# Optimization experiments

Measured on AMD Instinct MI355X. Metric: run time of the kernel, lower is better.

Reference implementation:

```python
import jax, jax.numpy as jnp
import numpy as np

B, C, H, W = 8, 512, 64, 64
K = 8  # shrink factor: qk channels = C//K, v channels = C//2


def conv1x1(x, w, b):
    # x: [B,C_in,H,W], w: [C_out,C_in], b: [C_out]  (1x1 conv == channel matmul)
    return jnp.einsum('bchw,oc->bohw', x, w) + b[None, :, None, None]


def maxpool2x2(x):
    b, c, h, w = x.shape
    return x.reshape(b, c, h // 2, 2, w // 2, 2).max(axis=(3, 5))


def setup_inputs() -> dict:
    key = jax.random.key(0)
    ks = jax.random.split(key, 9)
    Cqk, Cv = C // K, C // 2
    sc = lambda fan_in: 1.0 / np.sqrt(fan_in)
    return {
        'x': jax.random.normal(ks[0], (B, C, H, W), jnp.float32),
        'Wf': jax.random.normal(ks[1], (Cqk, C), jnp.float32) * sc(C),
        'bf': jnp.zeros((Cqk,), jnp.float32),
        'Wg': jax.random.normal(ks[2], (Cqk, C), jnp.float32) * sc(C),
        'bg': jnp.zeros((Cqk,), jnp.float32),
        'Wh': jax.random.normal(ks[3], (Cv, C), jnp.float32) * sc(C),
        'bh': jnp.zeros((Cv,), jnp.float32),
        'Wv': jax.random.normal(ks[4], (C, Cv), jnp.float32) * sc(Cv),
        'bv': jnp.zeros((C,), jnp.float32),
        'gamma': jnp.float32(0.5),
    }


def reference(x, Wf, bf, Wg, bg, Wh, bh, Wv, bv, gamma):
    b, c, h, w = x.shape
    f = conv1x1(x, Wf, bf).reshape(b, c // K, h * w)          # [B, C/K, HW]
    g = maxpool2x2(conv1x1(x, Wg, bg))                         # [B, C/K, H/2, W/2]
    v = maxpool2x2(conv1x1(x, Wh, bh))                         # [B, C/2, H/2, W/2]
    hwp = (h // 2) * (w // 2)
    g = g.reshape(b, c // K, hwp)
    v = v.reshape(b, c // 2, hwp)
    # s[b, n, m] = sum_c f[b,c,n] g[b,c,m]; softmax over m (no scaling, per SAGAN)
    s = jnp.einsum('bcn,bcm->bnm', f, g)                       # [B, HW, HW']
    beta = jax.nn.softmax(s, axis=-1)
    o = jnp.einsum('bcm,bnm->bcn', v, beta).reshape(b, c // 2, h, w)
    return gamma * conv1x1(o, Wv, bv) + x
```

## Files before the change

kernel.cpp:

```cpp
#include <hip/hip_runtime.h>
#include <cstddef>

typedef __attribute__((ext_vector_type(4))) float f32x4;
typedef __attribute__((ext_vector_type(16))) float f32x16;
typedef __attribute__((ext_vector_type(8))) short bf16x8;

#define MFMA16(A, B, C) __builtin_amdgcn_mfma_f32_16x16x32_bf16(A, B, C, 0, 0, 0)
#define MFMA32(A, B, C) __builtin_amdgcn_mfma_f32_32x32x16_bf16(A, B, C, 0, 0, 0)

__device__ __forceinline__ unsigned short f2bf(float f) {
  unsigned u = __float_as_uint(f);
  u += 0x7fffu + ((u >> 16) & 1u);
  return (unsigned short)(u >> 16);
}
__device__ __forceinline__ float bf2f(unsigned short s) {
  return __uint_as_float(((unsigned)s) << 16);
}

__device__ __forceinline__ void cvt_split8(float4 a, float4 b, bf16x8* H, bf16x8* L) {
  float v[8] = {a.x, a.y, a.z, a.w, b.x, b.y, b.z, b.w};
  unsigned hh[4], ll[4];
  #pragma unroll
  for (int p = 0; p < 4; ++p) {
    unsigned short h0 = f2bf(v[2 * p]), h1 = f2bf(v[2 * p + 1]);
    hh[p] = (unsigned)h0 | ((unsigned)h1 << 16);
    unsigned short l0 = f2bf(v[2 * p] - bf2f(h0));
    unsigned short l1 = f2bf(v[2 * p + 1] - bf2f(h1));
    ll[p] = (unsigned)l0 | ((unsigned)l1 << 16);
  }
  uint4 uh; uh.x = hh[0]; uh.y = hh[1]; uh.z = hh[2]; uh.w = hh[3];
  uint4 ul; ul.x = ll[0]; ul.y = ll[1]; ul.z = ll[2]; ul.w = ll[3];
  *H = *(bf16x8*)&uh;
  *L = *(bf16x8*)&ul;
}

__device__ __forceinline__ bf16x8 cvt_hi8(float4 a, float4 b) {
  float v[8] = {a.x, a.y, a.z, a.w, b.x, b.y, b.z, b.w};
  unsigned hh[4];
  #pragma unroll
  for (int p = 0; p < 4; ++p)
    hh[p] = (unsigned)f2bf(v[2 * p]) | ((unsigned)f2bf(v[2 * p + 1]) << 16);
  uint4 uh; uh.x = hh[0]; uh.y = hh[1]; uh.z = hh[2]; uh.w = hh[3];
  return *(bf16x8*)&uh;
}


__global__ void prep_k(const float* __restrict__ Wf, const float* __restrict__ Wg,
                       const float* __restrict__ Wh, const float* __restrict__ Wv,
                       unsigned short* __restrict__ wfh, unsigned short* __restrict__ wfl,
                       unsigned short* __restrict__ wgh, unsigned short* __restrict__ wgl,
                       unsigned short* __restrict__ whb, unsigned short* __restrict__ wvb) {
  int i = blockIdx.x * 256 + threadIdx.x;
  if (i < 65536) {
    int ii = i & 32767;
    int j = ii & 7, slot = (ii >> 3) & 63, q = slot & 15, qt2 = slot >> 4;
    int kt = (ii >> 9) & 15, oct = ii >> 13;
    const float* src = (i < 32768) ? Wf : Wg;
    unsigned short* dh = (i < 32768) ? wfh : wgh;
    unsigned short* dl = (i < 32768) ? wfl : wgl;
    float v = src[(oct * 16 + q) * 512 + kt * 32 + qt2 * 8 + j];
    unsigned short h = f2bf(v);
    dh[ii] = h; dl[ii] = f2bf(v - bf2f(h));
  } else if (i < 196608) {
    int ii = i - 65536;
    int j = ii & 7, slot = (ii >> 3) & 63, q = slot & 15, qt2 = slot >> 4;
    int kt = (ii >> 9) & 15, oct = ii >> 13;
    whb[ii] = f2bf(Wh[(oct * 16 + q) * 512 + kt * 32 + qt2 * 8 + j]);
  } else if (i < 327680) {
    int ii = i - 196608;
    int j = ii & 7, slot = (ii >> 3) & 63, q = slot & 15, qt2 = slot >> 4;
    int kt = (ii >> 9) & 7, oct = ii >> 12;
    wvb[ii] = f2bf(Wv[(oct * 16 + q) * 256 + kt * 32 + qt2 * 8 + j]);
  }
}


#define LOADX(CN) { _Pragma("unroll") \
  for (int t_ = 0; t_ < 16; ++t_) vv[t_] = xbase[(size_t)((CN) * 32 + kq + t_) * 4096]; }
#define STOREX(XS) { _Pragma("unroll") \
  for (int i_ = 0; i_ < 4; ++i_) { \
    float4 wv_; wv_.x = vv[4*i_]; wv_.y = vv[4*i_+1]; wv_.z = vv[4*i_+2]; wv_.w = vv[4*i_+3]; \
    *(float4*)&(XS)[nloc][kq + 4 * i_] = wv_; } }

__global__ __launch_bounds__(256, 2)
void conv_all(const float* __restrict__ x,
              const unsigned short* __restrict__ wfh_, const unsigned short* __restrict__ wfl_,
              const unsigned short* __restrict__ wgh_, const unsigned short* __restrict__ wgl_,
              const unsigned short* __restrict__ whb_,
              const float* __restrict__ bf_, const float* __restrict__ bg_,
              const float* __restrict__ bh_,
              unsigned short* __restrict__ fhi, unsigned short* __restrict__ flo,
              unsigned short* __restrict__ ghi, unsigned short* __restrict__ glo,
              unsigned short* __restrict__ vp)
{
  __shared__ __align__(16) char smem[34304];
  float (*xsA)[33] = (float(*)[33])smem;
  float (*xsB)[33] = (float(*)[33])(smem + 16896);
  const int bid = blockIdx.x;
  const int b = bid & 7;
  const int idx = bid >> 3;
  const int role = idx & 1;
  const int hp = idx >> 1;
  const int n0 = hp * 128;
  const int tid = threadIdx.x, w = tid >> 6, lane = tid & 63, q = lane & 15, qt = lane >> 4;
  const int nloc = tid & 127;
  const int kq = (tid >> 7) * 16;
  const float* xbase = x + (size_t)(b * 512) * 4096 + n0 + nloc;
  float vv[16];

  if (role == 0) {
    f32x4 accf[2][4], accg[2][4];
    #pragma unroll
    for (int nt = 0; nt < 2; ++nt)
      #pragma unroll
      for (int ot = 0; ot < 4; ++ot) {
        accf[nt][ot] = (f32x4){0.f, 0.f, 0.f, 0.f};
        accg[nt][ot] = (f32x4){0.f, 0.f, 0.f, 0.f};
      }
    LOADX(0) STOREX(xsA)
    __syncthreads();
    for (int cc = 0; cc < 16; ++cc) {
      float (*cur)[33] = (cc & 1) ? xsB : xsA;
      float (*nxt)[33] = (cc & 1) ? xsA : xsB;
      if (cc < 15) LOADX(cc + 1)
      bf16x8 Ah[2], Al[2];
      #pragma unroll
      for (int nt = 0; nt < 2; ++nt) {
        int row = w * 32 + nt * 16 + q;
        float4 a0 = *(const float4*)&cur[row][qt * 8];
        float4 a1 = *(const float4*)&cur[row][qt * 8 + 4];
        cvt_split8(a0, a1, &Ah[nt], &Al[nt]);
      }
      {
        bf16x8 Bh[4], Bl[4];
        #pragma unroll
        for (int ot = 0; ot < 4; ++ot) {
          size_t wb = ((size_t)(ot * 16 + cc) << 9) + lane * 8;
          Bh[ot] = *(const bf16x8*)(wfh_ + wb);
          Bl[ot] = *(const bf16x8*)(wfl_ + wb);
        }
        #pragma unroll
        for (int nt = 0; nt < 2; ++nt)
          #pragma unroll
          for (int ot = 0; ot < 4; ++ot) {
            accf[nt][ot] = MFMA16(Ah[nt], Bh[ot], accf[nt][ot]);
            accf[nt][ot] = MFMA16(Ah[nt], Bl[ot], accf[nt][ot]);
            accf[nt][ot] = MFMA16(Al[nt], Bh[ot], accf[nt][ot]);
          }
      }
      {
        bf16x8 Bh[4], Bl[4];
        #pragma unroll
        for (int ot = 0; ot < 4; ++ot) {
          size_t wb = ((size_t)(ot * 16 + cc) << 9) + lane * 8;
          Bh[ot] = *(const bf16x8*)(wgh_ + wb);
          Bl[ot] = *(const bf16x8*)(wgl_ + wb);
        }
        #pragma unroll
        for (int nt = 0; nt < 2; ++nt)
          #pragma unroll
          for (int ot = 0; ot < 4; ++ot) {
            accg[nt][ot] = MFMA16(Ah[nt], Bh[ot], accg[nt][ot]);
            accg[nt][ot] = MFMA16(Ah[nt], Bl[ot], accg[nt][ot]);
            accg[nt][ot] = MFMA16(Al[nt], Bh[ot], accg[nt][ot]);
          }
      }
      if (cc < 15) STOREX(nxt)
      __syncthreads();
    }
    #pragma unroll
    for (int nt = 0; nt < 2; ++nt)
      #pragma unroll
      for (int ot = 0; ot < 4; ++ot)
        #pragma unroll
        for (int r = 0; r < 4; ++r) {
          float v = accf[nt][ot][r] + bf_[ot * 16 + q];
          unsigned short h = f2bf(v);
          size_t o = (((size_t)(b * 128 + hp * 4 + w) * 4 + ot) * 64 +
                      (q >> 3) * 32 + nt * 16 + qt * 4 + r) * 8 + (q & 7);
          fhi[o] = h;
          flo[o] = f2bf(v - bf2f(h));
        }
    float (*pl)[67] = (float(*)[67])smem;
    #pragma unroll
    for (int nt = 0; nt < 2; ++nt)
      #pragma unroll
      for (int ot = 0; ot < 4; ++ot)
        #pragma unroll
        for (int r = 0; r < 4; ++r)
          pl[w * 32 + nt * 16 + qt * 4 + r][ot * 16 + q] = accg[nt][ot][r];
    __syncthreads();
    const int c = tid & 63;
    #pragma unroll
    for (int it = 0; it < 8; ++it) {
      int wp = (tid >> 6) + it * 4;
      float v = fmaxf(fmaxf(pl[2 * wp][c], pl[2 * wp + 1][c]),
                      fmaxf(pl[64 + 2 * wp][c], pl[65 + 2 * wp][c])) + bg_[c];
      unsigned short h = f2bf(v);
      size_t o = (((size_t)(b * 32 + hp) * 4 + (c >> 4)) * 64 +
                  ((c >> 3) & 1) * 32 + wp) * 8 + (c & 7);
      ghi[o] = h;
      glo[o] = f2bf(v - bf2f(h));
    }
  } else {
    f32x4 acc[2][16];
    #pragma unroll
    for (int nt = 0; nt < 2; ++nt)
      #pragma unroll
      for (int ot = 0; ot < 16; ++ot) acc[nt][ot] = (f32x4){0.f, 0.f, 0.f, 0.f};
    LOADX(0) STOREX(xsA)
    __syncthreads();
    for (int cc = 0; cc < 16; ++cc) {
      float (*cur)[33] = (cc & 1) ? xsB : xsA;
      float (*nxt)[33] = (cc & 1) ? xsA : xsB;
      if (cc < 15) LOADX(cc + 1)
      bf16x8 A_[2];
      #pragma unroll
      for (int nt = 0; nt < 2; ++nt) {
        int row = w * 32 + nt * 16 + q;
        float4 a0 = *(const float4*)&cur[row][qt * 8];
        float4 a1 = *(const float4*)&cur[row][qt * 8 + 4];
        A_[nt] = cvt_hi8(a0, a1);
      }
      #pragma unroll
      for (int oh = 0; oh < 2; ++oh) {
        bf16x8 B_[8];
        #pragma unroll
        for (int ot = 0; ot < 8; ++ot)
          B_[ot] = *(const bf16x8*)(whb_ + ((size_t)((oh * 8 + ot) * 16 + cc) << 9) + lane * 8);
        #pragma unroll
        for (int nt = 0; nt < 2; ++nt)
          #pragma unroll
          for (int ot = 0; ot < 8; ++ot)
            acc[nt][oh * 8 + ot] = MFMA16(A_[nt], B_[ot], acc[nt][oh * 8 + ot]);
      }
      if (cc < 15) STOREX(nxt)
      __syncthreads();
    }
    float (*pl)[67] = (float(*)[67])smem;
    #pragma unroll
    for (int oh = 0; oh < 4; ++oh) {
      if (oh) __syncthreads();
      #pragma unroll
      for (int nt = 0; nt < 2; ++nt)
        #pragma unroll
        for (int ot4 = 0; ot4 < 4; ++ot4)
          #pragma unroll
          for (int r = 0; r < 4; ++r)
            pl[w * 32 + nt * 16 + qt * 4 + r][ot4 * 16 + q] = acc[nt][oh * 4 + ot4][r];
      __syncthreads();
      const int wp = tid & 31;
      #pragma unroll
      for (int it = 0; it < 8; ++it) {
        int cc2 = (tid >> 5) + it * 8;
        int cv = oh * 64 + cc2;
        float v = fmaxf(fmaxf(pl[2 * wp][cc2], pl[2 * wp + 1][cc2]),
                        fmaxf(pl[64 + 2 * wp][cc2], pl[65 + 2 * wp][cc2])) + bh_[cv];
        size_t o = (((size_t)(b * 16 + (cv >> 4)) * 32 + hp) * 64 +
                    (wp >> 3) * 16 + (cv & 15)) * 8 + (wp & 7);
        vp[o] = f2bf(v);
      }
    }
  }
}


#define PROW 264

__global__ __launch_bounds__(256, 2)
void attn_mfma(const unsigned short* __restrict__ f_, const unsigned short* __restrict__ fl_,
               const unsigned short* __restrict__ g_, const unsigned short* __restrict__ gl_,
               const unsigned short* __restrict__ vp, unsigned short* __restrict__ oT)
{
  __shared__ __align__(16) unsigned short PB[64 * PROW];
  __shared__ float redm[4][2][32], reds[4][2][32];
  __shared__ float rfrow[64], Srow[64];
  const int b = blockIdx.x & 7, bx = blockIdx.x >> 3;
  const int tid = threadIdx.x, w = tid >> 6, lane = tid & 63;
  const int q32 = lane & 31, hl = lane >> 5;
  const int q16 = lane & 15, qt = lane >> 4;

  bf16x8 Fh[2][4], Fl[2][4];
  #pragma unroll
  for (int qt2 = 0; qt2 < 2; ++qt2) {
    size_t fb = ((size_t)(b * 128 + bx * 2 + qt2) << 11) + lane * 8;
    #pragma unroll
    for (int s = 0; s < 4; ++s) {
      Fh[qt2][s] = *(const bf16x8*)(f_ + fb + (s << 9));
      Fl[qt2][s] = *(const bf16x8*)(fl_ + fb + (s << 9));
    }
  }

  float M0 = -3.0e38f, M1 = -3.0e38f;
  f32x4 oacc[4][4];
  #pragma unroll
  for (int c4 = 0; c4 < 4; ++c4)
    #pragma unroll
    for (int qs = 0; qs < 4; ++qs) oacc[c4][qs] = (f32x4){0.f, 0.f, 0.f, 0.f};
  const size_t vroot = ((size_t)(b * 16 + w * 4) * 32) * 512 + lane * 8;

#define VLD(C4, KS) (*(const bf16x8*)(vp + vroot + ((size_t)((C4) * 32 + mc * 8 + (KS)) << 9)))
#define LOADVA(KS) { va0 = VLD(0, KS); va1 = VLD(1, KS); va2 = VLD(2, KS); va3 = VLD(3, KS); }
#define LOADVB(KS) { vb0 = VLD(0, KS); vb1 = VLD(1, KS); vb2 = VLD(2, KS); vb3 = VLD(3, KS); }
#define PVMFMA(KS, V0, V1, V2, V3) { \
  bf16x8 pb0 = *(const bf16x8*)&PB[q16 * PROW + (KS) * 32 + qt * 8]; \
  bf16x8 pb1 = *(const bf16x8*)&PB[(16 + q16) * PROW + (KS) * 32 + qt * 8]; \
  bf16x8 pb2 = *(const bf16x8*)&PB[(32 + q16) * PROW + (KS) * 32 + qt * 8]; \
  bf16x8 pb3 = *(const bf16x8*)&PB[(48 + q16) * PROW + (KS) * 32 + qt * 8]; \
  oacc[0][0] = MFMA16(V0, pb0, oacc[0][0]); oacc[1][0] = MFMA16(V1, pb0, oacc[1][0]); \
  oacc[2][0] = MFMA16(V2, pb0, oacc[2][0]); oacc[3][0] = MFMA16(V3, pb0, oacc[3][0]); \
  oacc[0][1] = MFMA16(V0, pb1, oacc[0][1]); oacc[1][1] = MFMA16(V1, pb1, oacc[1][1]); \
  oacc[2][1] = MFMA16(V2, pb1, oacc[2][1]); oacc[3][1] = MFMA16(V3, pb1, oacc[3][1]); \
  oacc[0][2] = MFMA16(V0, pb2, oacc[0][2]); oacc[1][2] = MFMA16(V1, pb2, oacc[1][2]); \
  oacc[2][2] = MFMA16(V2, pb2, oacc[2][2]); oacc[3][2] = MFMA16(V3, pb2, oacc[3][2]); \
  oacc[0][3] = MFMA16(V0, pb3, oacc[0][3]); oacc[1][3] = MFMA16(V1, pb3, oacc[1][3]); \
  oacc[2][3] = MFMA16(V2, pb3, oacc[2][3]); oacc[3][3] = MFMA16(V3, pb3, oacc[3][3]); }

  #pragma unroll 1
  for (int mc = 0; mc < 4; ++mc) {
    f32x16 sa0t0 = {}, sa0t1 = {}, sa1t0 = {}, sa1t1 = {};
    #pragma unroll
    for (int t = 0; t < 2; ++t) {
      size_t gb = ((size_t)(b * 32 + mc * 8 + w * 2 + t) << 11) + lane * 8;
      bf16x8 Gh[4], Gl[4];
      #pragma unroll
      for (int s = 0; s < 4; ++s) {
        Gh[s] = *(const bf16x8*)(g_ + gb + (s << 9));
        Gl[s] = *(const bf16x8*)(gl_ + gb + (s << 9));
      }
      f32x16* s0 = t ? &sa0t1 : &sa0t0;
      f32x16* s1 = t ? &sa1t1 : &sa1t0;
      #pragma unroll
      for (int s = 0; s < 4; ++s) {
        *s0 = MFMA32(Gh[s], Fh[0][s], *s0);
        *s0 = MFMA32(Gh[s], Fl[0][s], *s0);
        *s0 = MFMA32(Gl[s], Fh[0][s], *s0);
        *s1 = MFMA32(Gh[s], Fh[1][s], *s1);
        *s1 = MFMA32(Gh[s], Fl[1][s], *s1);
        *s1 = MFMA32(Gl[s], Fh[1][s], *s1);
      }
    }

    bf16x8 va0, va1, va2, va3, vb0, vb1, vb2, vb3;
    LOADVA(0)

    float mx0 = -3.0e38f, mx1 = -3.0e38f;
    #pragma unroll
    for (int r = 0; r < 16; ++r) {
      mx0 = fmaxf(mx0, fmaxf(sa0t0[r], sa0t1[r]));
      mx1 = fmaxf(mx1, fmaxf(sa1t0[r], sa1t1[r]));
    }
    mx0 = fmaxf(mx0, __shfl_xor(mx0, 32));
    mx1 = fmaxf(mx1, __shfl_xor(mx1, 32));
    if (lane < 32) { redm[w][0][lane] = mx0; redm[w][1][lane] = mx1; }
    __syncthreads();
    float gmx0 = fmaxf(fmaxf(redm[0][0][q32], redm[1][0][q32]), fmaxf(redm[2][0][q32], redm[3][0][q32]));
    float gmx1 = fmaxf(fmaxf(redm[0][1][q32], redm[1][1][q32]), fmaxf(redm[2][1][q32], redm[3][1][q32]));
    float Mn0 = fmaxf(M0, gmx0), Mn1 = fmaxf(M1, gmx1);
    float rf0 = __expf(M0 - Mn0), rf1 = __expf(M1 - Mn1);
    M0 = Mn0; M1 = Mn1;
    float cs0 = 0.f, cs1 = 0.f;
    #pragma unroll
    for (int r = 0; r < 16; ++r) {
      float p;
      p = __expf(sa0t0[r] - Mn0); sa0t0[r] = p; cs0 += p;
      p = __expf(sa0t1[r] - Mn0); sa0t1[r] = p; cs0 += p;
      p = __expf(sa1t0[r] - Mn1); sa1t0[r] = p; cs1 += p;
      p = __expf(sa1t1[r] - Mn1); sa1t1[r] = p; cs1 += p;
    }
    cs0 += __shfl_xor(cs0, 32);
    cs1 += __shfl_xor(cs1, 32);
    if (lane < 32) { reds[w][0][lane] = cs0; reds[w][1][lane] = cs1; }

    #pragma unroll
    for (int j = 0; j < 4; ++j) {
      uint2 pk;
      pk.x = (unsigned)f2bf(sa0t0[4*j+0]) | ((unsigned)f2bf(sa0t0[4*j+1]) << 16);
      pk.y = (unsigned)f2bf(sa0t0[4*j+2]) | ((unsigned)f2bf(sa0t0[4*j+3]) << 16);
      *(uint2*)&PB[q32 * PROW + w * 64 + j * 8 + hl * 4] = pk;
      pk.x = (unsigned)f2bf(sa0t1[4*j+0]) | ((unsigned)f2bf(sa0t1[4*j+1]) << 16);
      pk.y = (unsigned)f2bf(sa0t1[4*j+2]) | ((unsigned)f2bf(sa0t1[4*j+3]) << 16);
      *(uint2*)&PB[q32 * PROW + w * 64 + 32 + j * 8 + hl * 4] = pk;
      pk.x = (unsigned)f2bf(sa1t0[4*j+0]) | ((unsigned)f2bf(sa1t0[4*j+1]) << 16);
      pk.y = (unsigned)f2bf(sa1t0[4*j+2]) | ((unsigned)f2bf(sa1t0[4*j+3]) << 16);
      *(uint2*)&PB[(32 + q32) * PROW + w * 64 + j * 8 + hl * 4] = pk;
      pk.x = (unsigned)f2bf(sa1t1[4*j+0]) | ((unsigned)f2bf(sa1t1[4*j+1]) << 16);
      pk.y = (unsigned)f2bf(sa1t1[4*j+2]) | ((unsigned)f2bf(sa1t1[4*j+3]) << 16);
      *(uint2*)&PB[(32 + q32) * PROW + w * 64 + 32 + j * 8 + hl * 4] = pk;
    }
    __syncthreads();
    float ct0 = reds[0][0][q32] + reds[1][0][q32] + reds[2][0][q32] + reds[3][0][q32];
    float ct1 = reds[0][1][q32] + reds[1][1][q32] + reds[2][1][q32] + reds[3][1][q32];
    if (w == 0 && lane < 32) {
      Srow[lane]      = (mc == 0) ? ct0 : Srow[lane]      * rf0 + ct0;
      Srow[32 + lane] = (mc == 0) ? ct1 : Srow[32 + lane] * rf1 + ct1;
      rfrow[lane] = rf0; rfrow[32 + lane] = rf1;
    }
    __syncthreads();

    if (mc > 0) {
      float rfq[4];
      #pragma unroll
      for (int qs = 0; qs < 4; ++qs) rfq[qs] = rfrow[qs * 16 + q16];
      #pragma unroll
      for (int c4 = 0; c4 < 4; ++c4)
        #pragma unroll
        for (int qs = 0; qs < 4; ++qs) oacc[c4][qs] *= rfq[qs];
    }
    LOADVB(1)
    #pragma unroll
    for (int kp = 0; kp < 4; ++kp) {
      PVMFMA(2 * kp, va0, va1, va2, va3)
      if (2 * kp + 2 < 8) LOADVA(2 * kp + 2)
      PVMFMA(2 * kp + 1, vb0, vb1, vb2, vb3)
      if (2 * kp + 3 < 8) LOADVB(2 * kp + 3)
    }
  }

  __syncthreads();
  float rinv[4];
  #pragma unroll
  for (int qs = 0; qs < 4; ++qs) rinv[qs] = 1.0f / Srow[qs * 16 + q16];
  #pragma unroll
  for (int c4 = 0; c4 < 4; ++c4)
    #pragma unroll
    for (int qs = 0; qs < 4; ++qs) {
      uint2 pk;
      pk.x = (unsigned)f2bf(oacc[c4][qs][0] * rinv[qs]) | ((unsigned)f2bf(oacc[c4][qs][1] * rinv[qs]) << 16);
      pk.y = (unsigned)f2bf(oacc[c4][qs][2] * rinv[qs]) | ((unsigned)f2bf(oacc[c4][qs][3] * rinv[qs]) << 16);
      *(uint2*)&PB[(qs * 16 + q16) * PROW + w * 64 + c4 * 16 + qt * 4] = pk;
    }
  __syncthreads();
  const size_t obase = (size_t)(b * 256 + bx * 4) * 4096;
  #pragma unroll
  for (int it = 0; it < 8; ++it) {
    int u = it * 256 + tid;
    int so = u * 8;
    int ntl = so >> 12;
    int rem = so & 4095;
    int ks = rem >> 9;
    int slot = (rem >> 3) & 63;
    int qq = slot & 15, cg = slot >> 4;
    uint4 val = *(const uint4*)&PB[(ntl * 16 + qq) * PROW + ks * 32 + cg * 8];
    *(uint4*)(oT + obase + so) = val;
  }
}


__global__ __launch_bounds__(256)
void conv_final(const unsigned short* __restrict__ A, const unsigned short* __restrict__ W,
                const float* __restrict__ bias, float* __restrict__ out,
                const float* __restrict__ resid, const float* __restrict__ gamma_p)
{
  const int bid = blockIdx.x;
  const int b = bid & 7;
  const int idx = bid >> 3;
  const int n0 = (idx & 31) * 128;
  const int oc0 = (idx >> 5) * 128;
  const int tid = threadIdx.x, w = tid >> 6, lane = tid & 63, q = lane & 15, qt = lane >> 4;

  f32x4 acc[2][8];
  #pragma unroll
  for (int nt = 0; nt < 2; ++nt)
    #pragma unroll
    for (int ot = 0; ot < 8; ++ot) acc[nt][ot] = (f32x4){0.f, 0.f, 0.f, 0.f};

  #pragma unroll
  for (int ks = 0; ks < 8; ++ks) {
    bf16x8 A_[2], B_[8];
    #pragma unroll
    for (int nt = 0; nt < 2; ++nt)
      A_[nt] = *(const bf16x8*)(A + (((size_t)(b * 256 + (n0 >> 4) + w * 2 + nt) * 8 + ks) << 9) + lane * 8);
    #pragma unroll
    for (int ot = 0; ot < 8; ++ot)
      B_[ot] = *(const bf16x8*)(W + (((size_t)((oc0 >> 4) + ot) * 8 + ks) << 9) + lane * 8);
    #pragma unroll
    for (int nt = 0; nt < 2; ++nt)
      #pragma unroll
      for (int ot = 0; ot < 8; ++ot)
        acc[nt][ot] = MFMA16(A_[nt], B_[ot], acc[nt][ot]);
  }

  const float gm = gamma_p[0];
  #pragma unroll
  for (int ot = 0; ot < 8; ++ot) {
    int oc = oc0 + ot * 16 + q;
    float bs = bias[oc];
    #pragma unroll
    for (int nt = 0; nt < 2; ++nt) {
      int n = n0 + w * 32 + nt * 16 + qt * 4;
      size_t o = ((size_t)(b * 512) + oc) * 4096 + n;
      float4 rs = *(const float4*)&resid[o];
      float4 ov;
      ov.x = gm * (acc[nt][ot][0] + bs) + rs.x;
      ov.y = gm * (acc[nt][ot][1] + bs) + rs.y;
      ov.z = gm * (acc[nt][ot][2] + bs) + rs.z;
      ov.w = gm * (acc[nt][ot][3] + bs) + rs.w;
      *(float4*)&out[o] = ov;
    }
  }
}


extern "C" void kernel_launch(void* const* d_in, const int* in_sizes, int n_in,
                              void* d_out, int out_size, void* d_ws, size_t ws_size,
                              hipStream_t stream) {
  const float* x     = (const float*)d_in[0];
  const float* Wf    = (const float*)d_in[1];
  const float* bf    = (const float*)d_in[2];
  const float* Wg    = (const float*)d_in[3];
  const float* bg    = (const float*)d_in[4];
  const float* Wh    = (const float*)d_in[5];
  const float* bh    = (const float*)d_in[6];
  const float* Wv    = (const float*)d_in[7];
  const float* bv    = (const float*)d_in[8];
  const float* gamma = (const float*)d_in[9];
  float* out = (float*)d_out;
  char* w = (char*)d_ws;

  unsigned short* fhi = (unsigned short*)(w);
  unsigned short* flo = (unsigned short*)(w + 4194304);
  unsigned short* ghi = (unsigned short*)(w + 8388608);
  unsigned short* glo = (unsigned short*)(w + 9437184);
  unsigned short* vp  = (unsigned short*)(w + 10485760);
  unsigned short* oT  = (unsigned short*)(w + 14680064);
  unsigned short* wfh = (unsigned short*)(w + 31457280);
  unsigned short* wfl = (unsigned short*)(w + 31522816);
  unsigned short* wgh = (unsigned short*)(w + 31588352);
  unsigned short* wgl = (unsigned short*)(w + 31653888);
  unsigned short* whb = (unsigned short*)(w + 31719424);
  unsigned short* wvb = (unsigned short*)(w + 31981568);

  prep_k<<<1280, 256, 0, stream>>>(Wf, Wg, Wh, Wv, wfh, wfl, wgh, wgl, whb, wvb);

  conv_all<<<512, 256, 0, stream>>>(x, wfh, wfl, wgh, wgl, whb,
                                    bf, bg, bh, fhi, flo, ghi, glo, vp);

  attn_mfma<<<512, 256, 0, stream>>>(fhi, flo, ghi, glo, vp, oT);

  conv_final<<<1024, 256, 0, stream>>>(oT, wvb, bv, out, x, gamma);
}
```

Before: 115.9 us.

## Double the conv K-chunk to 64 channels and raise wave priority around MFMA blocks

The conv kernel now stages 64 input channels per double-buffered LDS chunk instead of 32. That halves the number of outer iterations and barriers, and each thread loads 32 x values per step. The attention kernel wraps its QK and PV MFMA sections in s_setprio so those waves get issue priority. The cost is more registers (vv grows to 32 floats) and more LDS (about 66KB versus 34KB), which may hurt occupancy under launch_bounds(256,2).

After: 111.7 us. -3.6%, faster.

```diff
diff --git a/kernel.cpp b/kernel.cpp
--- a/kernel.cpp
+++ b/kernel.cpp
@@ -75,12 +75,12 @@
 }
 
 
-#define LOADX(CN) { _Pragma("unroll") \
-  for (int t_ = 0; t_ < 16; ++t_) vv[t_] = xbase[(size_t)((CN) * 32 + kq + t_) * 4096]; }
-#define STOREX(XS) { _Pragma("unroll") \
-  for (int i_ = 0; i_ < 4; ++i_) { \
+#define LOADX64(CN) { _Pragma("unroll") \
+  for (int t_ = 0; t_ < 32; ++t_) vv[t_] = xbase[(size_t)((CN) * 64 + kq + t_) * 4096]; }
+#define STOREX64(BUF) { _Pragma("unroll") \
+  for (int i_ = 0; i_ < 8; ++i_) { \
     float4 wv_; wv_.x = vv[4*i_]; wv_.y = vv[4*i_+1]; wv_.z = vv[4*i_+2]; wv_.w = vv[4*i_+3]; \
-    *(float4*)&(XS)[nloc][kq + 4 * i_] = wv_; } }
+    *(float4*)&xs[BUF][nloc][kq + 4 * i_] = wv_; } }
 
 __global__ __launch_bounds__(256, 2)
 void conv_all(const float* __restrict__ x,
@@ -93,9 +93,7 @@
               unsigned short* __restrict__ ghi, unsigned short* __restrict__ glo,
               unsigned short* __restrict__ vp)
 {
-  __shared__ __align__(16) char smem[34304];
-  float (*xsA)[33] = (float(*)[33])smem;
-  float (*xsB)[33] = (float(*)[33])(smem + 16896);
+  __shared__ __align__(16) float xs[2][128][65];
   const int bid = blockIdx.x;
   const int b = bid & 7;
   const int idx = bid >> 3;
@@ -104,9 +102,9 @@
   const int n0 = hp * 128;
   const int tid = threadIdx.x, w = tid >> 6, lane = tid & 63, q = lane & 15, qt = lane >> 4;
   const int nloc = tid & 127;
-  const int kq = (tid >> 7) * 16;
+  const int kq = (tid >> 7) * 32;
   const float* xbase = x + (size_t)(b * 512) * 4096 + n0 + nloc;
-  float vv[16];
+  float vv[32];
 
   if (role == 0) {
     f32x4 accf[2][4], accg[2][4];
@@ -117,55 +115,58 @@
         accf[nt][ot] = (f32x4){0.f, 0.f, 0.f, 0.f};
         accg[nt][ot] = (f32x4){0.f, 0.f, 0.f, 0.f};
       }
-    LOADX(0) STOREX(xsA)
+    LOADX64(0) STOREX64(0)
     __syncthreads();
-    for (int cc = 0; cc < 16; ++cc) {
-      float (*cur)[33] = (cc & 1) ? xsB : xsA;
-      float (*nxt)[33] = (cc & 1) ? xsA : xsB;
-      if (cc < 15) LOADX(cc + 1)
-      bf16x8 Ah[2], Al[2];
-      #pragma unroll
-      for (int nt = 0; nt < 2; ++nt) {
-        int row = w * 32 + nt * 16 + q;
-        float4 a0 = *(const float4*)&cur[row][qt * 8];
-        float4 a1 = *(const float4*)&cur[row][qt * 8 + 4];
-        cvt_split8(a0, a1, &Ah[nt], &Al[nt]);
+    for (int cc = 0; cc < 8; ++cc) {
+      const int cur = cc & 1;
+      if (cc < 7) LOADX64(cc + 1)
+      #pragma unroll
+      for (int kh = 0; kh < 2; ++kh) {
+        const int kt = cc * 2 + kh;
+        bf16x8 Ah[2], Al[2];
+        #pragma unroll
+        for (int nt = 0; nt < 2; ++nt) {
+          int row = w * 32 + nt * 16 + q;
+          float4 a0 = *(const float4*)&xs[cur][row][kh * 32 + qt * 8];
+          float4 a1 = *(const float4*)&xs[cur][row][kh * 32 + qt * 8 + 4];
+          cvt_split8(a0, a1, &Ah[nt], &Al[nt]);
+        }
+        {
+          bf16x8 Bh[4], Bl[4];
+          #pragma unroll
+          for (int ot = 0; ot < 4; ++ot) {
+            size_t wb = ((size_t)(ot * 16 + kt) << 9) + lane * 8;
+            Bh[ot] = *(const bf16x8*)(wfh_ + wb);
+            Bl[ot] = *(const bf16x8*)(wfl_ + wb);
+          }
+          #pragma unroll
+          for (int nt = 0; nt < 2; ++nt)
+            #pragma unroll
+            for (int ot = 0; ot < 4; ++ot) {
+              accf[nt][ot] = MFMA16(Ah[nt], Bh[ot], accf[nt][ot]);
+              accf[nt][ot] = MFMA16(Ah[nt], Bl[ot], accf[nt][ot]);
+              accf[nt][ot] = MFMA16(Al[nt], Bh[ot], accf[nt][ot]);
+            }
+        }
+        {
+          bf16x8 Bh[4], Bl[4];
+          #pragma unroll
+          for (int ot = 0; ot < 4; ++ot) {
+            size_t wb = ((size_t)(ot * 16 + kt) << 9) + lane * 8;
+            Bh[ot] = *(const bf16x8*)(wgh_ + wb);
+            Bl[ot] = *(const bf16x8*)(wgl_ + wb);
+          }
+          #pragma unroll
+          for (int nt = 0; nt < 2; ++nt)
+            #pragma unroll
+            for (int ot = 0; ot < 4; ++ot) {
+              accg[nt][ot] = MFMA16(Ah[nt], Bh[ot], accg[nt][ot]);
+              accg[nt][ot] = MFMA16(Ah[nt], Bl[ot], accg[nt][ot]);
+              accg[nt][ot] = MFMA16(Al[nt], Bh[ot], accg[nt][ot]);
+            }
+        }
       }
-      {
-        bf16x8 Bh[4], Bl[4];
-        #pragma unroll
-        for (int ot = 0; ot < 4; ++ot) {
-          size_t wb = ((size_t)(ot * 16 + cc) << 9) + lane * 8;
-          Bh[ot] = *(const bf16x8*)(wfh_ + wb);
-          Bl[ot] = *(const bf16x8*)(wfl_ + wb);
-        }
-        #pragma unroll
-        for (int nt = 0; nt < 2; ++nt)
-          #pragma unroll
-          for (int ot = 0; ot < 4; ++ot) {
-            accf[nt][ot] = MFMA16(Ah[nt], Bh[ot], accf[nt][ot]);
-            accf[nt][ot] = MFMA16(Ah[nt], Bl[ot], accf[nt][ot]);
-            accf[nt][ot] = MFMA16(Al[nt], Bh[ot], accf[nt][ot]);
-          }
-      }
-      {
-        bf16x8 Bh[4], Bl[4];
-        #pragma unroll
-        for (int ot = 0; ot < 4; ++ot) {
-          size_t wb = ((size_t)(ot * 16 + cc) << 9) + lane * 8;
-          Bh[ot] = *(const bf16x8*)(wgh_ + wb);
-          Bl[ot] = *(const bf16x8*)(wgl_ + wb);
-        }
-        #pragma unroll
-        for (int nt = 0; nt < 2; ++nt)
-          #pragma unroll
-          for (int ot = 0; ot < 4; ++ot) {
-            accg[nt][ot] = MFMA16(Ah[nt], Bh[ot], accg[nt][ot]);
-            accg[nt][ot] = MFMA16(Ah[nt], Bl[ot], accg[nt][ot]);
-            accg[nt][ot] = MFMA16(Al[nt], Bh[ot], accg[nt][ot]);
-          }
-      }
-      if (cc < 15) STOREX(nxt)
+      if (cc < 7) STOREX64(cur ^ 1)
       __syncthreads();
     }
     #pragma unroll
@@ -181,7 +182,7 @@
           fhi[o] = h;
           flo[o] = f2bf(v - bf2f(h));
         }
-    float (*pl)[67] = (float(*)[67])smem;
+    float (*pl)[67] = (float(*)[67])&xs[0][0][0];
     #pragma unroll
     for (int nt = 0; nt < 2; ++nt)
       #pragma unroll
@@ -208,36 +209,39 @@
     for (int nt = 0; nt < 2; ++nt)
       #pragma unroll
       for (int ot = 0; ot < 16; ++ot) acc[nt][ot] = (f32x4){0.f, 0.f, 0.f, 0.f};
-    LOADX(0) STOREX(xsA)
+    LOADX64(0) STOREX64(0)
     __syncthreads();
-    for (int cc = 0; cc < 16; ++cc) {
-      float (*cur)[33] = (cc & 1) ? xsB : xsA;
-      float (*nxt)[33] = (cc & 1) ? xsA : xsB;
-      if (cc < 15) LOADX(cc + 1)
-      bf16x8 A_[2];
-      #pragma unroll
-      for (int nt = 0; nt < 2; ++nt) {
-        int row = w * 32 + nt * 16 + q;
-        float4 a0 = *(const float4*)&cur[row][qt * 8];
-        float4 a1 = *(const float4*)&cur[row][qt * 8 + 4];
-        A_[nt] = cvt_hi8(a0, a1);
+    for (int cc = 0; cc < 8; ++cc) {
+      const int cur = cc & 1;
+      if (cc < 7) LOADX64(cc + 1)
+      #pragma unroll
+      for (int kh = 0; kh < 2; ++kh) {
+        const int kt = cc * 2 + kh;
+        bf16x8 A_[2];
+        #pragma unroll
+        for (int nt = 0; nt < 2; ++nt) {
+          int row = w * 32 + nt * 16 + q;
+          float4 a0 = *(const float4*)&xs[cur][row][kh * 32 + qt * 8];
+          float4 a1 = *(const float4*)&xs[cur][row][kh * 32 + qt * 8 + 4];
+          A_[nt] = cvt_hi8(a0, a1);
+        }
+        #pragma unroll
+        for (int oh = 0; oh < 2; ++oh) {
+          bf16x8 B_[8];
+          #pragma unroll
+          for (int ot = 0; ot < 8; ++ot)
+            B_[ot] = *(const bf16x8*)(whb_ + ((size_t)((oh * 8 + ot) * 16 + kt) << 9) + lane * 8);
+          #pragma unroll
+          for (int nt = 0; nt < 2; ++nt)
+            #pragma unroll
+            for (int ot = 0; ot < 8; ++ot)
+              acc[nt][oh * 8 + ot] = MFMA16(A_[nt], B_[ot], acc[nt][oh * 8 + ot]);
+        }
       }
-      #pragma unroll
-      for (int oh = 0; oh < 2; ++oh) {
-        bf16x8 B_[8];
-        #pragma unroll
-        for (int ot = 0; ot < 8; ++ot)
-          B_[ot] = *(const bf16x8*)(whb_ + ((size_t)((oh * 8 + ot) * 16 + cc) << 9) + lane * 8);
-        #pragma unroll
-        for (int nt = 0; nt < 2; ++nt)
-          #pragma unroll
-          for (int ot = 0; ot < 8; ++ot)
-            acc[nt][oh * 8 + ot] = MFMA16(A_[nt], B_[ot], acc[nt][oh * 8 + ot]);
-      }
-      if (cc < 15) STOREX(nxt)
+      if (cc < 7) STOREX64(cur ^ 1)
       __syncthreads();
     }
-    float (*pl)[67] = (float(*)[67])smem;
+    float (*pl)[67] = (float(*)[67])&xs[0][0][0];
     #pragma unroll
     for (int oh = 0; oh < 4; ++oh) {
       if (oh) __syncthreads();
@@ -319,6 +323,7 @@
   #pragma unroll 1
   for (int mc = 0; mc < 4; ++mc) {
     f32x16 sa0t0 = {}, sa0t1 = {}, sa1t0 = {}, sa1t1 = {};
+    __builtin_amdgcn_s_setprio(1);
     #pragma unroll
     for (int t = 0; t < 2; ++t) {
       size_t gb = ((size_t)(b * 32 + mc * 8 + w * 2 + t) << 11) + lane * 8;
@@ -340,6 +345,7 @@
         *s1 = MFMA32(Gl[s], Fh[1][s], *s1);
       }
     }
+    __builtin_amdgcn_s_setprio(0);
 
     bf16x8 va0, va1, va2, va3, vb0, vb1, vb2, vb3;
     LOADVA(0)
@@ -408,6 +414,7 @@
         for (int qs = 0; qs < 4; ++qs) oacc[c4][qs] *= rfq[qs];
     }
     LOADVB(1)
+    __builtin_amdgcn_s_setprio(1);
     #pragma unroll
     for (int kp = 0; kp < 4; ++kp) {
       PVMFMA(2 * kp, va0, va1, va2, va3)
@@ -415,6 +422,7 @@
       PVMFMA(2 * kp + 1, vb0, vb1, vb2, vb3)
       if (2 * kp + 3 < 8) LOADVB(2 * kp + 3)
     }
+    __builtin_amdgcn_s_setprio(0);
   }
 
   __syncthreads();
```

## Merge conv roles into 512-thread blocks sharing x tiles, pool in registers

Applied to the files above, without the earlier changes.

The conv kernel now runs f/g and v roles as two halves of one 512-thread block, so each x tile is loaded once and shared instead of being read by two separate blocks. K-chunks double to 64 with register double-buffering. Warp rows are remapped so each thread's accumulators hold the 2x2 pooling window, which removes the LDS transpose and the extra barriers in the max-pool epilogue. s_setprio hints are added around the MFMA bursts in both conv and attention. The costs are higher register pressure from two 16-float staging buffers and a larger LDS footprint per block, which may lower occupancy.

New measurement: 122.3 us. 5.5% more time.

```diff
diff --git a/kernel.cpp b/kernel.cpp
--- a/kernel.cpp
+++ b/kernel.cpp
@@ -75,14 +75,16 @@
 }
 
 
-#define LOADX(CN) { _Pragma("unroll") \
-  for (int t_ = 0; t_ < 16; ++t_) vv[t_] = xbase[(size_t)((CN) * 32 + kq + t_) * 4096]; }
-#define STOREX(XS) { _Pragma("unroll") \
+#define SPX 65
+
+#define LOADV(V, CN) { _Pragma("unroll") \
+  for (int t_ = 0; t_ < 16; ++t_) V[t_] = xbase[(size_t)((CN) * 64 + kq + t_) * 4096]; }
+#define STOREV(V, BUF) { _Pragma("unroll") \
   for (int i_ = 0; i_ < 4; ++i_) { \
-    float4 wv_; wv_.x = vv[4*i_]; wv_.y = vv[4*i_+1]; wv_.z = vv[4*i_+2]; wv_.w = vv[4*i_+3]; \
-    *(float4*)&(XS)[nloc][kq + 4 * i_] = wv_; } }
-
-__global__ __launch_bounds__(256, 2)
+    float4 wv_; wv_.x = V[4*i_]; wv_.y = V[4*i_+1]; wv_.z = V[4*i_+2]; wv_.w = V[4*i_+3]; \
+    *(float4*)&xs[BUF][nloc][kq + 4 * i_] = wv_; } }
+
+__global__ __launch_bounds__(512, 2)
 void conv_all(const float* __restrict__ x,
               const unsigned short* __restrict__ wfh_, const unsigned short* __restrict__ wfl_,
               const unsigned short* __restrict__ wgh_, const unsigned short* __restrict__ wgl_,
@@ -93,20 +95,20 @@
               unsigned short* __restrict__ ghi, unsigned short* __restrict__ glo,
               unsigned short* __restrict__ vp)
 {
-  __shared__ __align__(16) char smem[34304];
-  float (*xsA)[33] = (float(*)[33])smem;
-  float (*xsB)[33] = (float(*)[33])(smem + 16896);
+  __shared__ __align__(16) float xs[2][128][SPX];
   const int bid = blockIdx.x;
   const int b = bid & 7;
-  const int idx = bid >> 3;
-  const int role = idx & 1;
-  const int hp = idx >> 1;
+  const int hp = bid >> 3;
   const int n0 = hp * 128;
   const int tid = threadIdx.x, w = tid >> 6, lane = tid & 63, q = lane & 15, qt = lane >> 4;
+  const int wl = w & 3;
+  const int role = w >> 2;
   const int nloc = tid & 127;
   const int kq = (tid >> 7) * 16;
+  const int rowA = wl * 16 + q;
+  const int rowB = 64 + rowA;
   const float* xbase = x + (size_t)(b * 512) * 4096 + n0 + nloc;
-  float vv[16];
+  float vvA[16], vvB[16];
 
   if (role == 0) {
     f32x4 accf[2][4], accg[2][4];
@@ -117,57 +119,64 @@
         accf[nt][ot] = (f32x4){0.f, 0.f, 0.f, 0.f};
         accg[nt][ot] = (f32x4){0.f, 0.f, 0.f, 0.f};
       }
-    LOADX(0) STOREX(xsA)
+    LOADV(vvA, 0) STOREV(vvA, 0) LOADV(vvA, 1)
     __syncthreads();
-    for (int cc = 0; cc < 16; ++cc) {
-      float (*cur)[33] = (cc & 1) ? xsB : xsA;
-      float (*nxt)[33] = (cc & 1) ? xsA : xsB;
-      if (cc < 15) LOADX(cc + 1)
-      bf16x8 Ah[2], Al[2];
-      #pragma unroll
-      for (int nt = 0; nt < 2; ++nt) {
-        int row = w * 32 + nt * 16 + q;
-        float4 a0 = *(const float4*)&cur[row][qt * 8];
-        float4 a1 = *(const float4*)&cur[row][qt * 8 + 4];
-        cvt_split8(a0, a1, &Ah[nt], &Al[nt]);
-      }
-      {
-        bf16x8 Bh[4], Bl[4];
-        #pragma unroll
-        for (int ot = 0; ot < 4; ++ot) {
-          size_t wb = ((size_t)(ot * 16 + cc) << 9) + lane * 8;
-          Bh[ot] = *(const bf16x8*)(wfh_ + wb);
-          Bl[ot] = *(const bf16x8*)(wfl_ + wb);
-        }
-        #pragma unroll
-        for (int nt = 0; nt < 2; ++nt)
-          #pragma unroll
-          for (int ot = 0; ot < 4; ++ot) {
-            accf[nt][ot] = MFMA16(Ah[nt], Bh[ot], accf[nt][ot]);
-            accf[nt][ot] = MFMA16(Ah[nt], Bl[ot], accf[nt][ot]);
-            accf[nt][ot] = MFMA16(Al[nt], Bh[ot], accf[nt][ot]);
-          }
-      }
-      {
-        bf16x8 Bh[4], Bl[4];
-        #pragma unroll
-        for (int ot = 0; ot < 4; ++ot) {
-          size_t wb = ((size_t)(ot * 16 + cc) << 9) + lane * 8;
-          Bh[ot] = *(const bf16x8*)(wgh_ + wb);
-          Bl[ot] = *(const bf16x8*)(wgl_ + wb);
-        }
-        #pragma unroll
-        for (int nt = 0; nt < 2; ++nt)
-          #pragma unroll
-          for (int ot = 0; ot < 4; ++ot) {
-            accg[nt][ot] = MFMA16(Ah[nt], Bh[ot], accg[nt][ot]);
-            accg[nt][ot] = MFMA16(Ah[nt], Bl[ot], accg[nt][ot]);
-            accg[nt][ot] = MFMA16(Al[nt], Bh[ot], accg[nt][ot]);
-          }
-      }
-      if (cc < 15) STOREX(nxt)
+
+#define COMPUTE_FG(BUF, CC) { \
+    _Pragma("unroll") \
+    for (int kh = 0; kh < 2; ++kh) { \
+      const int kt = (CC) * 2 + kh; \
+      bf16x8 Ah[2], Al[2]; \
+      { float4 a0 = *(const float4*)&xs[BUF][rowA][kh * 32 + qt * 8]; \
+        float4 a1 = *(const float4*)&xs[BUF][rowA][kh * 32 + qt * 8 + 4]; \
+        cvt_split8(a0, a1, &Ah[0], &Al[0]); } \
+      { float4 a0 = *(const float4*)&xs[BUF][rowB][kh * 32 + qt * 8]; \
+        float4 a1 = *(const float4*)&xs[BUF][rowB][kh * 32 + qt * 8 + 4]; \
+        cvt_split8(a0, a1, &Ah[1], &Al[1]); } \
+      { bf16x8 Bh[4], Bl[4]; \
+        _Pragma("unroll") \
+        for (int ot = 0; ot < 4; ++ot) { \
+          size_t wb = ((size_t)(ot * 16 + kt) << 9) + lane * 8; \
+          Bh[ot] = *(const bf16x8*)(wfh_ + wb); \
+          Bl[ot] = *(const bf16x8*)(wfl_ + wb); } \
+        __builtin_amdgcn_s_setprio(1); \
+        _Pragma("unroll") \
+        for (int nt = 0; nt < 2; ++nt) \
+          _Pragma("unroll") \
+          for (int ot = 0; ot < 4; ++ot) { \
+            accf[nt][ot] = MFMA16(Ah[nt], Bh[ot], accf[nt][ot]); \
+            accf[nt][ot] = MFMA16(Ah[nt], Bl[ot], accf[nt][ot]); \
+            accf[nt][ot] = MFMA16(Al[nt], Bh[ot], accf[nt][ot]); } \
+        __builtin_amdgcn_s_setprio(0); } \
+      { bf16x8 Bh[4], Bl[4]; \
+        _Pragma("unroll") \
+        for (int ot = 0; ot < 4; ++ot) { \
+          size_t wb = ((size_t)(ot * 16 + kt) << 9) + lane * 8; \
+          Bh[ot] = *(const bf16x8*)(wgh_ + wb); \
+          Bl[ot] = *(const bf16x8*)(wgl_ + wb); } \
+        __builtin_amdgcn_s_setprio(1); \
+        _Pragma("unroll") \
+        for (int nt = 0; nt < 2; ++nt) \
+          _Pragma("unroll") \
+          for (int ot = 0; ot < 4; ++ot) { \
+            accg[nt][ot] = MFMA16(Ah[nt], Bh[ot], accg[nt][ot]); \
+            accg[nt][ot] = MFMA16(Ah[nt], Bl[ot], accg[nt][ot]); \
+            accg[nt][ot] = MFMA16(Al[nt], Bh[ot], accg[nt][ot]); } \
+        __builtin_amdgcn_s_setprio(0); } \
+    } }
+
+    #pragma unroll
+    for (int cp = 0; cp < 4; ++cp) {
+      if (cp < 3) LOADV(vvB, 2 * cp + 2)
+      COMPUTE_FG(0, 2 * cp)
+      STOREV(vvA, 1)
       __syncthreads();
-    }
+      if (cp < 3) LOADV(vvA, 2 * cp + 3)
+      COMPUTE_FG(1, 2 * cp + 1)
+      if (cp < 3) STOREV(vvB, 0)
+      __syncthreads();
+    }
+
     #pragma unroll
     for (int nt = 0; nt < 2; ++nt)
       #pragma unroll
@@ -176,31 +185,27 @@
         for (int r = 0; r < 4; ++r) {
           float v = accf[nt][ot][r] + bf_[ot * 16 + q];
           unsigned short h = f2bf(v);
-          size_t o = (((size_t)(b * 128 + hp * 4 + w) * 4 + ot) * 64 +
-                      (q >> 3) * 32 + nt * 16 + qt * 4 + r) * 8 + (q & 7);
+          int grp = hp * 4 + nt * 2 + (wl >> 1);
+          int ing = (wl & 1) * 16 + qt * 4 + r;
+          size_t o = (((size_t)(b * 128 + grp) * 4 + ot) * 64 +
+                      (q >> 3) * 32 + ing) * 8 + (q & 7);
           fhi[o] = h;
           flo[o] = f2bf(v - bf2f(h));
         }
-    float (*pl)[67] = (float(*)[67])smem;
-    #pragma unroll
-    for (int nt = 0; nt < 2; ++nt)
-      #pragma unroll
-      for (int ot = 0; ot < 4; ++ot)
-        #pragma unroll
-        for (int r = 0; r < 4; ++r)
-          pl[w * 32 + nt * 16 + qt * 4 + r][ot * 16 + q] = accg[nt][ot][r];
-    __syncthreads();
-    const int c = tid & 63;
-    #pragma unroll
-    for (int it = 0; it < 8; ++it) {
-      int wp = (tid >> 6) + it * 4;
-      float v = fmaxf(fmaxf(pl[2 * wp][c], pl[2 * wp + 1][c]),
-                      fmaxf(pl[64 + 2 * wp][c], pl[65 + 2 * wp][c])) + bg_[c];
-      unsigned short h = f2bf(v);
-      size_t o = (((size_t)(b * 32 + hp) * 4 + (c >> 4)) * 64 +
-                  ((c >> 3) & 1) * 32 + wp) * 8 + (c & 7);
-      ghi[o] = h;
-      glo[o] = f2bf(v - bf2f(h));
+    #pragma unroll
+    for (int ot = 0; ot < 4; ++ot) {
+      float bsv = bg_[ot * 16 + q];
+      #pragma unroll
+      for (int u = 0; u < 2; ++u) {
+        float v = fmaxf(fmaxf(accg[0][ot][2 * u], accg[0][ot][2 * u + 1]),
+                        fmaxf(accg[1][ot][2 * u], accg[1][ot][2 * u + 1])) + bsv;
+        unsigned short h = f2bf(v);
+        int wp = wl * 8 + qt * 2 + u;
+        size_t o = (((size_t)(b * 32 + hp) * 4 + ot) * 64 +
+                    (q >> 3) * 32 + wp) * 8 + (q & 7);
+        ghi[o] = h;
+        glo[o] = f2bf(v - bf2f(h));
+      }
     }
   } else {
     f32x4 acc[2][16];
@@ -208,58 +213,61 @@
     for (int nt = 0; nt < 2; ++nt)
       #pragma unroll
       for (int ot = 0; ot < 16; ++ot) acc[nt][ot] = (f32x4){0.f, 0.f, 0.f, 0.f};
-    LOADX(0) STOREX(xsA)
+    LOADV(vvA, 0) STOREV(vvA, 0) LOADV(vvA, 1)
     __syncthreads();
-    for (int cc = 0; cc < 16; ++cc) {
-      float (*cur)[33] = (cc & 1) ? xsB : xsA;
-      float (*nxt)[33] = (cc & 1) ? xsA : xsB;
-      if (cc < 15) LOADX(cc + 1)
-      bf16x8 A_[2];
-      #pragma unroll
-      for (int nt = 0; nt < 2; ++nt) {
-        int row = w * 32 + nt * 16 + q;
-        float4 a0 = *(const float4*)&cur[row][qt * 8];
-        float4 a1 = *(const float4*)&cur[row][qt * 8 + 4];
-        A_[nt] = cvt_hi8(a0, a1);
+
+#define COMPUTE_V(BUF, CC) { \
+    _Pragma("unroll") \
+    for (int kh = 0; kh < 2; ++kh) { \
+      const int kt = (CC) * 2 + kh; \
+      bf16x8 A_[2]; \
+      { float4 a0 = *(const float4*)&xs[BUF][rowA][kh * 32 + qt * 8]; \
+        float4 a1 = *(const float4*)&xs[BUF][rowA][kh * 32 + qt * 8 + 4]; \
+        A_[0] = cvt_hi8(a0, a1); } \
+      { float4 a0 = *(const float4*)&xs[BUF][rowB][kh * 32 + qt * 8]; \
+        float4 a1 = *(const float4*)&xs[BUF][rowB][kh * 32 + qt * 8 + 4]; \
+        A_[1] = cvt_hi8(a0, a1); } \
+      _Pragma("unroll") \
+      for (int oh = 0; oh < 2; ++oh) { \
+        bf16x8 B_[8]; \
+        _Pragma("unroll") \
+        for (int ot = 0; ot < 8; ++ot) \
+          B_[ot] = *(const bf16x8*)(whb_ + ((size_t)((oh * 8 + ot) * 16 + kt) << 9) + lane * 8); \
+        __builtin_amdgcn_s_setprio(1); \
+        _Pragma("unroll") \
+        for (int nt = 0; nt < 2; ++nt) \
+          _Pragma("unroll") \
+          for (int ot = 0; ot < 8; ++ot) \
+            acc[nt][oh * 8 + ot] = MFMA16(A_[nt], B_[ot], acc[nt][oh * 8 + ot]); \
+        __builtin_amdgcn_s_setprio(0); \
+      } \
+    } }
+
+    #pragma unroll
+    for (int cp = 0; cp < 4; ++cp) {
+      if (cp < 3) LOADV(vvB, 2 * cp + 2)
+      COMPUTE_V(0, 2 * cp)
+      STOREV(vvA, 1)
+      __syncthreads();
+      if (cp < 3) LOADV(vvA, 2 * cp + 3)
+      COMPUTE_V(1, 2 * cp + 1)
+      if (cp < 3) STOREV(vvB, 0)
+      __syncthreads();
+    }
+
+    #pragma unroll
+    for (int ot = 0; ot < 16; ++ot) {
+      float bsv = bh_[ot * 16 + q];
+      unsigned short hs[2];
+      #pragma unroll
+      for (int u = 0; u < 2; ++u) {
+        float v = fmaxf(fmaxf(acc[0][ot][2 * u], acc[0][ot][2 * u + 1]),
+                        fmaxf(acc[1][ot][2 * u], acc[1][ot][2 * u + 1])) + bsv;
+        hs[u] = f2bf(v);
       }
-      #pragma unroll
-      for (int oh = 0; oh < 2; ++oh) {
-        bf16x8 B_[8];
-        #pragma unroll
-        for (int ot = 0; ot < 8; ++ot)
-          B_[ot] = *(const bf16x8*)(whb_ + ((size_t)((oh * 8 + ot) * 16 + cc) << 9) + lane * 8);
-        #pragma unroll
-        for (int nt = 0; nt < 2; ++nt)
-          #pragma unroll
-          for (int ot = 0; ot < 8; ++ot)
-            acc[nt][oh * 8 + ot] = MFMA16(A_[nt], B_[ot], acc[nt][oh * 8 + ot]);
-      }
-      if (cc < 15) STOREX(nxt)
-      __syncthreads();
-    }
-    float (*pl)[67] = (float(*)[67])smem;
-    #pragma unroll
-    for (int oh = 0; oh < 4; ++oh) {
-      if (oh) __syncthreads();
-      #pragma unroll
-      for (int nt = 0; nt < 2; ++nt)
-        #pragma unroll
-        for (int ot4 = 0; ot4 < 4; ++ot4)
-          #pragma unroll
-          for (int r = 0; r < 4; ++r)
-            pl[w * 32 + nt * 16 + qt * 4 + r][ot4 * 16 + q] = acc[nt][oh * 4 + ot4][r];
-      __syncthreads();
-      const int wp = tid & 31;
-      #pragma unroll
-      for (int it = 0; it < 8; ++it) {
-        int cc2 = (tid >> 5) + it * 8;
-        int cv = oh * 64 + cc2;
-        float v = fmaxf(fmaxf(pl[2 * wp][cc2], pl[2 * wp + 1][cc2]),
-                        fmaxf(pl[64 + 2 * wp][cc2], pl[65 + 2 * wp][cc2])) + bh_[cv];
-        size_t o = (((size_t)(b * 16 + (cv >> 4)) * 32 + hp) * 64 +
-                    (wp >> 3) * 16 + (cv & 15)) * 8 + (wp & 7);
-        vp[o] = f2bf(v);
-      }
+      unsigned pk = (unsigned)hs[0] | ((unsigned)hs[1] << 16);
+      size_t o = (((size_t)(b * 16 + ot) * 32 + hp) * 64 + wl * 16 + q) * 8 + qt * 2;
+      *(unsigned*)(vp + o) = pk;
     }
   }
 }
@@ -319,6 +327,7 @@
   #pragma unroll 1
   for (int mc = 0; mc < 4; ++mc) {
     f32x16 sa0t0 = {}, sa0t1 = {}, sa1t0 = {}, sa1t1 = {};
+    __builtin_amdgcn_s_setprio(1);
     #pragma unroll
     for (int t = 0; t < 2; ++t) {
       size_t gb = ((size_t)(b * 32 + mc * 8 + w * 2 + t) << 11) + lane * 8;
@@ -340,6 +349,7 @@
         *s1 = MFMA32(Gl[s], Fh[1][s], *s1);
       }
     }
+    __builtin_amdgcn_s_setprio(0);
 
     bf16x8 va0, va1, va2, va3, vb0, vb1, vb2, vb3;
     LOADVA(0)
@@ -408,6 +418,7 @@
         for (int qs = 0; qs < 4; ++qs) oacc[c4][qs] *= rfq[qs];
     }
     LOADVB(1)
+    __builtin_amdgcn_s_setprio(1);
     #pragma unroll
     for (int kp = 0; kp < 4; ++kp) {
       PVMFMA(2 * kp, va0, va1, va2, va3)
@@ -415,6 +426,7 @@
       PVMFMA(2 * kp + 1, vb0, vb1, vb2, vb3)
       if (2 * kp + 3 < 8) LOADVB(2 * kp + 3)
     }
+    __builtin_amdgcn_s_setprio(0);
   }
 
   __syncthreads();
@@ -533,7 +545,7 @@
 
   prep_k<<<1280, 256, 0, stream>>>(Wf, Wg, Wh, Wv, wfh, wfl, wgh, wgl, whb, wvb);
 
-  conv_all<<<512, 256, 0, stream>>>(x, wfh, wfl, wgh, wgl, whb,
+  conv_all<<<256, 512, 0, stream>>>(x, wfh, wfl, wgh, wgl, whb,
                                     bf, bg, bh, fhi, flo, ghi, glo, vp);
 
   attn_mfma<<<512, 256, 0, stream>>>(fhi, flo, ghi, glo, vp, oT);
```
